# Optimization experiments

Measured on AMD Instinct MI355X. Metric: run time of the kernel, lower is better.

## Reference

```python
import jax, jax.numpy as jnp
import numpy as np

PAD = 1  # symmetric spatial padding (pad_H == pad_W enforced by the module)


def setup_inputs() -> dict:
    key = jax.random.key(0)
    k1, k2, k3 = jax.random.split(key, 3)
    N, C, F, H, W, HH, WW = 32, 128, 128, 32, 32, 3, 3
    x = jax.random.normal(k1, (N, C, H, W), dtype=jnp.float32)
    weight = jax.random.normal(k2, (F, C, HH, WW), dtype=jnp.float32) * 0.05
    bias = jax.random.normal(k3, (F,), dtype=jnp.float32) * 0.05
    return {"x": x, "weight": weight, "bias": bias}


def reference(x, weight, bias):
    # Conv2dfft forward, no compression (compress_rate=0, preserve_energy=100,
    # next_power2=False, stride=1, real_fft path).
    N, C, H, W = x.shape
    F, _, HH, WW = weight.shape
    pad = PAD
    out_H = H - HH + 1 + 2 * pad
    out_W = W - WW + 1 + 2 * pad
    HHH = max(out_H, HH)
    WWW = max(out_W, WW)
    init_H = H + 2 * pad + HHH - 1  # full linear-conv FFT size
    init_W = W + 2 * pad + WWW - 1
    # torch_pad(input, (pad_W, pad_W + fft_pad_W, pad_H, pad_H + fft_pad_H))
    xp = jnp.pad(x, ((0, 0), (0, 0), (pad, init_H - pad - H), (pad, init_W - pad - W)))
    # torch_pad(filter, (0, fft_pad_W, 0, fft_pad_H))
    wp = jnp.pad(weight, ((0, 0), (0, 0), (0, init_H - HH), (0, init_W - WW)))
    xf = jnp.fft.rfft2(xp)          # [N, C, init_H, init_W//2+1] complex
    wf = jnp.fft.rfft2(wp)          # [F, C, init_H, init_W//2+1] complex
    # Cross-correlation in frequency domain: xfft * conj(yfft), contracted
    # over input channels C per frequency bin. This is exactly the math of the
    # module's fast_multiply (3-real-mult complex product via matmul) applied
    # to the conjugated filter spectrum.
    of = jnp.einsum('nchw,fchw->nfhw', xf, jnp.conj(wf))
    out = jnp.fft.irfft2(of, s=(init_H, init_W))[..., :out_H, :out_W]
    return out + bias[None, :, None, None]
```

## Files before the change

### kernel.cpp

```cpp
#include <hip/hip_runtime.h>


typedef short bf16x8 __attribute__((ext_vector_type(8)));
typedef float f32x4  __attribute__((ext_vector_type(4)));

__device__ __forceinline__ short f2bf(float f) {
  unsigned u = __builtin_bit_cast(unsigned, f);
  u = (u + 0x7fffu + ((u >> 16) & 1u)) >> 16;
  return (short)u;
}

__device__ __forceinline__ void gload_lds16(const void* g, void* l) {
  __builtin_amdgcn_global_load_lds(
      (const __attribute__((address_space(1))) unsigned int*)g,
      (__attribute__((address_space(3))) unsigned int*)l,
      16, 0, 0);
}

__global__ __launch_bounds__(256) void conv_wprep(const float* __restrict__ w,
                                                  short* __restrict__ bc) {
  int tid = blockIdx.x * 256 + threadIdx.x;
  int ci  = tid & 31;
  int f   = (tid >> 5) & 127;
  int grp = tid >> 12;
  int pq  = grp % 9;
  int chunk = grp / 9;
  int p = pq / 3, q = pq % 3;
  int c = chunk * 32 + ci;
  float v = w[((f * 128 + c) * 3 + p) * 3 + q];
  bc[(grp * 128 + f) * 40 + ci] = f2bf(v);
}

__global__ __launch_bounds__(256, 1) void conv_main(
    const float* __restrict__ x, const short* __restrict__ bc,
    const float* __restrict__ bias, float* __restrict__ out) {
  __shared__ __align__(16) short ws[3 * 128 * 40];
  __shared__ __align__(16) short xs[6 * 34 * 40];

  const int t    = threadIdx.x;
  const int lane = t & 63;
  const int wv   = t >> 6;
  const int n_img = blockIdx.x >> 3;
  const int h0    = (blockIdx.x & 7) << 2;

  const int l15  = lane & 15;
  const int quad = lane >> 4;
  const int f_off  = (wv & 1) * 64;
  const int s_rowb = (wv >> 1) * 2;

  if (t < 192) {
    int r = t >> 5, ci = t & 31;
    xs[(r * 34 + 0)  * 40 + ci] = 0;
    xs[(r * 34 + 33) * 40 + ci] = 0;
  }

  f32x4 acc[4][4] = {};

  const int w_ = t & 31;
  const int g  = t >> 5;
  const float* xb = x + ((n_img * 128) * 32 + (h0 - 1)) * 32 + w_;

  for (int chunk = 0; chunk < 4; ++chunk) {
    const int c0 = chunk * 32;
#pragma unroll
    for (int i = 0; i < 24; ++i) {
      int comb = i * 8 + g;
      int r = comb >> 5, ci = comb & 31;
      int hr = h0 - 1 + r;
      float v = 0.f;
      if (hr >= 0 && hr < 32) v = xb[(c0 + ci) * 1024 + r * 32];
      xs[(r * 34 + (w_ + 1)) * 40 + ci] = f2bf(v);
    }
#pragma unroll
    for (int p = 0; p < 3; ++p) {
      const char* src = (const char*)bc + (chunk * 3 + p) * 30720;
      for (int i = wv; i < 30; i += 4)
        gload_lds16(src + i * 1024 + lane * 16, (char*)ws + i * 1024);
      __syncthreads();
#pragma unroll
      for (int q = 0; q < 3; ++q) {
        bf16x8 af[4], bfr[4];
#pragma unroll
        for (int mt = 0; mt < 4; ++mt)
          af[mt] = *(const bf16x8*)&ws[(q * 128 + f_off + mt * 16 + l15) * 40 + quad * 8];
#pragma unroll
        for (int nt = 0; nt < 4; ++nt) {
          int r_out = s_rowb + (nt >> 1);
          int w_out = (nt & 1) * 16 + l15;
          bfr[nt] = *(const bf16x8*)&xs[((r_out + p) * 34 + w_out + q) * 40 + quad * 8];
        }
#pragma unroll
        for (int mt = 0; mt < 4; ++mt)
#pragma unroll
          for (int nt = 0; nt < 4; ++nt)
            acc[mt][nt] = __builtin_amdgcn_mfma_f32_16x16x32_bf16(
                af[mt], bfr[nt], acc[mt][nt], 0, 0, 0);
      }
      __syncthreads();
    }
  }

#pragma unroll
  for (int nt = 0; nt < 4; ++nt) {
    int h = h0 + s_rowb + (nt >> 1);
    int w_out = (nt & 1) * 16 + l15;
#pragma unroll
    for (int mt = 0; mt < 4; ++mt) {
#pragma unroll
      for (int reg = 0; reg < 4; ++reg) {
        int f = f_off + mt * 16 + quad * 4 + reg;
        out[((n_img * 128 + f) * 32 + h) * 32 + w_out] = acc[mt][nt][reg] + bias[f];
      }
    }
  }
}

extern "C" void kernel_launch(void* const* d_in, const int* in_sizes, int n_in,
                              void* d_out, int out_size, void* d_ws, size_t ws_size,
                              hipStream_t stream) {
  const float* x    = (const float*)d_in[0];
  const float* w    = (const float*)d_in[1];
  const float* bias = (const float*)d_in[2];
  float* out = (float*)d_out;
  short* bc  = (short*)d_ws;

  conv_wprep<<<576, 256, 0, stream>>>(w, bc);
  conv_main<<<256, 256, 0, stream>>>(x, bc, bias, out);
}
```

Baseline: 98.90 us.

## Double-buffer input tile in LDS and read pre-swizzled weights directly from global

Weights are pre-laid-out by the prep kernel in exact MFMA fragment order, so the main kernel loads A fragments straight from global/L2 instead of staging them through LDS with per-tap barriers. The input tile is double-buffered in LDS, with the next channel chunk prefetched into registers during compute and written as packed bf16x4 stores. This cuts barriers from two per row-tap to one per chunk and overlaps global loads with MFMA work, at the cost of more registers and global weight traffic per wave.

```diff
diff --git a/kernel.cpp b/kernel.cpp
--- a/kernel.cpp
+++ b/kernel.cpp
@@ -2,6 +2,7 @@
 
 
 typedef short bf16x8 __attribute__((ext_vector_type(8)));
+typedef short bf16x4 __attribute__((ext_vector_type(4)));
 typedef float f32x4  __attribute__((ext_vector_type(4)));
 
 __device__ __forceinline__ short f2bf(float f) {
@@ -10,32 +11,25 @@
   return (short)u;
 }
 
-__device__ __forceinline__ void gload_lds16(const void* g, void* l) {
-  __builtin_amdgcn_global_load_lds(
-      (const __attribute__((address_space(1))) unsigned int*)g,
-      (__attribute__((address_space(3))) unsigned int*)l,
-      16, 0, 0);
-}
-
 __global__ __launch_bounds__(256) void conv_wprep(const float* __restrict__ w,
-                                                  short* __restrict__ bc) {
-  int tid = blockIdx.x * 256 + threadIdx.x;
-  int ci  = tid & 31;
-  int f   = (tid >> 5) & 127;
-  int grp = tid >> 12;
-  int pq  = grp % 9;
-  int chunk = grp / 9;
-  int p = pq / 3, q = pq % 3;
-  int c = chunk * 32 + ci;
-  float v = w[((f * 128 + c) * 3 + p) * 3 + q];
-  bc[(grp * 128 + f) * 40 + ci] = f2bf(v);
+                                                  short* __restrict__ bc2) {
+  int tid  = blockIdx.x * 256 + threadIdx.x;
+  int j    = tid & 7;
+  int l15  = (tid >> 3) & 15;
+  int quad = (tid >> 7) & 3;
+  int fblk = (tid >> 9) & 7;
+  int g2   = tid >> 12;
+  int chunk = g2 / 9, tap = g2 % 9;
+  int p = tap / 3, q = tap % 3;
+  int f = fblk * 16 + l15;
+  int c = chunk * 32 + quad * 8 + j;
+  bc2[tid] = f2bf(w[(f * 128 + c) * 9 + p * 3 + q]);
 }
 
 __global__ __launch_bounds__(256, 1) void conv_main(
-    const float* __restrict__ x, const short* __restrict__ bc,
+    const float* __restrict__ x, const short* __restrict__ bc2,
     const float* __restrict__ bias, float* __restrict__ out) {
-  __shared__ __align__(16) short ws[3 * 128 * 40];
-  __shared__ __align__(16) short xs[6 * 34 * 40];
+  __shared__ __align__(16) short xs[2][6 * 34 * 36];
 
   const int t    = threadIdx.x;
   const int lane = t & 63;
@@ -48,46 +42,64 @@
   const int f_off  = (wv & 1) * 64;
   const int s_rowb = (wv >> 1) * 2;
 
+  const int w_ = t & 31;
+  const int g  = t >> 5;
+  const float* xb = x + n_img * 128 * 1024;
+
   if (t < 192) {
-    int r = t >> 5, ci = t & 31;
-    xs[(r * 34 + 0)  * 40 + ci] = 0;
-    xs[(r * 34 + 33) * 40 + ci] = 0;
+    int buf = t / 96, rem = t % 96;
+    int r = rem / 16, rem2 = rem % 16;
+    int colsel = rem2 / 8, q4 = rem2 % 8;
+    *(int2*)&xs[buf][(r * 34 + colsel * 33) * 36 + q4 * 4] = make_int2(0, 0);
   }
 
   f32x4 acc[4][4] = {};
+  float xv[24];
 
-  const int w_ = t & 31;
-  const int g  = t >> 5;
-  const float* xb = x + ((n_img * 128) * 32 + (h0 - 1)) * 32 + w_;
+#pragma unroll
+  for (int r = 0; r < 6; ++r) {
+    int hr = h0 - 1 + r;
+    bool ok = (unsigned)hr < 32u;
+#pragma unroll
+    for (int cc = 0; cc < 4; ++cc)
+      xv[r * 4 + cc] = ok ? xb[((g * 4 + cc) * 32 + hr) * 32 + w_] : 0.f;
+  }
+#pragma unroll
+  for (int r = 0; r < 6; ++r) {
+    bf16x4 v = { f2bf(xv[r*4+0]), f2bf(xv[r*4+1]), f2bf(xv[r*4+2]), f2bf(xv[r*4+3]) };
+    *(bf16x4*)&xs[0][(r * 34 + w_ + 1) * 36 + g * 4] = v;
+  }
+  __syncthreads();
 
+#pragma unroll
   for (int chunk = 0; chunk < 4; ++chunk) {
-    const int c0 = chunk * 32;
+    if (chunk < 3) {
 #pragma unroll
-    for (int i = 0; i < 24; ++i) {
-      int comb = i * 8 + g;
-      int r = comb >> 5, ci = comb & 31;
-      int hr = h0 - 1 + r;
-      float v = 0.f;
-      if (hr >= 0 && hr < 32) v = xb[(c0 + ci) * 1024 + r * 32];
-      xs[(r * 34 + (w_ + 1)) * 40 + ci] = f2bf(v);
+      for (int r = 0; r < 6; ++r) {
+        int hr = h0 - 1 + r;
+        bool ok = (unsigned)hr < 32u;
+#pragma unroll
+        for (int cc = 0; cc < 4; ++cc)
+          xv[r * 4 + cc] =
+              ok ? xb[(((chunk + 1) * 32 + g * 4 + cc) * 32 + hr) * 32 + w_] : 0.f;
+      }
     }
+    const short* xbuf = xs[chunk & 1];
 #pragma unroll
     for (int p = 0; p < 3; ++p) {
-      const char* src = (const char*)bc + (chunk * 3 + p) * 30720;
-      for (int i = wv; i < 30; i += 4)
-        gload_lds16(src + i * 1024 + lane * 16, (char*)ws + i * 1024);
-      __syncthreads();
 #pragma unroll
       for (int q = 0; q < 3; ++q) {
+        const int tap = p * 3 + q;
+        const short* wb = bc2 + ((chunk * 9 + tap) * 8 + (wv & 1) * 4) * 512;
         bf16x8 af[4], bfr[4];
 #pragma unroll
         for (int mt = 0; mt < 4; ++mt)
-          af[mt] = *(const bf16x8*)&ws[(q * 128 + f_off + mt * 16 + l15) * 40 + quad * 8];
+          af[mt] = *(const bf16x8*)&wb[mt * 512 + lane * 8];
 #pragma unroll
         for (int nt = 0; nt < 4; ++nt) {
-          int r_out = s_rowb + (nt >> 1);
-          int w_out = (nt & 1) * 16 + l15;
-          bfr[nt] = *(const bf16x8*)&xs[((r_out + p) * 34 + w_out + q) * 40 + quad * 8];
+          int r   = s_rowb + (nt >> 1) + p;
+          int col = (nt & 1) * 16 + l15 + q;
+          bfr[nt] = *(const bf16x8*)&xbuf[(r * 34 + col) * 36 + quad * 8];
         }
 #pragma unroll
         for (int mt = 0; mt < 4; ++mt)
@@ -95,6 +107,13 @@
           for (int nt = 0; nt < 4; ++nt)
             acc[mt][nt] = __builtin_amdgcn_mfma_f32_16x16x32_bf16(
                 af[mt], bfr[nt], acc[mt][nt], 0, 0, 0);
+      }
+    }
+    if (chunk < 3) {
+#pragma unroll
+      for (int r = 0; r < 6; ++r) {
+        bf16x4 v = { f2bf(xv[r*4+0]), f2bf(xv[r*4+1]), f2bf(xv[r*4+2]), f2bf(xv[r*4+3]) };
+        *(bf16x4*)&xs[(chunk + 1) & 1][(r * 34 + w_ + 1) * 36 + g * 4] = v;
       }
       __syncthreads();
     }
@@ -122,8 +141,8 @@
   const float* w    = (const float*)d_in[1];
   const float* bias = (const float*)d_in[2];
   float* out = (float*)d_out;
-  short* bc  = (short*)d_ws;
+  short* bc2 = (short*)d_ws;
 
-  conv_wprep<<<576, 256, 0, stream>>>(w, bc);
-  conv_main<<<256, 256, 0, stream>>>(x, bc, bias, out);
+  conv_wprep<<<576, 256, 0, stream>>>(w, bc2);
+  conv_main<<<256, 256, 0, stream>>>(x, bc2, bias, out);
 }
```

After: 95.41 us. -3.5%, faster.
